# Optimization experiments

Hardware: AMD Instinct MI355X
Metric: run time of the kernel (lower is better)

## Reference

```python
import jax, jax.numpy as jnp
import numpy as np

H = 200  # LSTM units per layer
SEQ_LEN = 100
NUM_AXIS = 4


def setup_inputs() -> dict:
    key = jax.random.key(0)
    ks = jax.random.split(key, 12)
    B = 8192
    s = 0.05  # small init scale to avoid gate saturation
    inp = {
        "x": jax.random.normal(ks[0], (B, SEQ_LEN, 1), dtype=jnp.float32),
        # layer 0: input dim 1
        "W0": jax.random.normal(ks[1], (1, 4 * H), dtype=jnp.float32) * s,
        "U0": jax.random.normal(ks[2], (H, 4 * H), dtype=jnp.float32) * s,
        "b0": jax.random.normal(ks[3], (4 * H,), dtype=jnp.float32) * s,
        # layer 1
        "W1": jax.random.normal(ks[4], (H, 4 * H), dtype=jnp.float32) * s,
        "U1": jax.random.normal(ks[5], (H, 4 * H), dtype=jnp.float32) * s,
        "b1": jax.random.normal(ks[6], (4 * H,), dtype=jnp.float32) * s,
        # layer 2
        "W2": jax.random.normal(ks[7], (H, 4 * H), dtype=jnp.float32) * s,
        "U2": jax.random.normal(ks[8], (H, 4 * H), dtype=jnp.float32) * s,
        "b2": jax.random.normal(ks[9], (4 * H,), dtype=jnp.float32) * s,
        # dense head: 200 -> 400, tanh
        "Wfc": jax.random.normal(ks[10], (H, SEQ_LEN * NUM_AXIS), dtype=jnp.float32) * s,
        "bfc": jax.random.normal(ks[11], (SEQ_LEN * NUM_AXIS,), dtype=jnp.float32) * s,
    }
    return inp


def _lstm_step(h, c, xt, W, U, b):
    # Keras LSTMCell gate order: i, f, g(candidate), o
    z = xt @ W + h @ U + b  # [B, 4H]
    i, f, g, o = jnp.split(z, 4, axis=-1)
    c_new = jax.nn.sigmoid(f) * c + jax.nn.sigmoid(i) * jnp.tanh(g)
    h_new = jax.nn.sigmoid(o) * jnp.tanh(c_new)
    return h_new, c_new


def reference(x, W0, U0, b0, W1, U1, b1, W2, U2, b2, Wfc, bfc):
    B = x.shape[0]
    zeros = jnp.zeros((B, H), dtype=x.dtype)
    carry0 = (zeros, zeros, zeros, zeros, zeros, zeros)

    def step(carry, xt):
        h0, c0, h1, c1, h2, c2 = carry
        h0, c0 = _lstm_step(h0, c0, xt, W0, U0, b0)
        h1, c1 = _lstm_step(h1, c1, h0, W1, U1, b1)
        h2, c2 = _lstm_step(h2, c2, h1, W2, U2, b2)
        return (h0, c0, h1, c1, h2, c2), None

    # scan over time: x is [B, T, 1] -> [T, B, 1]
    xs = jnp.swapaxes(x, 0, 1)
    (h0, c0, h1, c1, h2, c2), _ = jax.lax.scan(step, carry0, xs)
    # return_sequences=False -> final top-layer hidden state
    y = jnp.tanh(h2 @ Wfc + bfc)  # [B, 400]
    return y.reshape(B, SEQ_LEN, NUM_AXIS)
```

## Files before the change

### kernel.cpp

```cpp
#include <hip/hip_runtime.h>

#define Hdim 200
#define NP   800
#define Tlen 100
#define BT   32
#define KB   7
#define HS   232
#define NT   50
#define THREADS 640
#define CH   5
#define CHSTR (NT*64*8)
#define MATSZ (KB*CHSTR)
#define SBUF  2560

#define WAIT_VM0   0x0F70
#define WAIT_VM5   0x0F75
#define WAIT_LGKM0 0xC07F

typedef float f32x4 __attribute__((ext_vector_type(4)));
typedef short s16x8 __attribute__((ext_vector_type(8)));

__device__ __forceinline__ ushort f2bf(float f) {
    unsigned u = __float_as_uint(f);
    return (ushort)((u + 0x7fffu + ((u >> 16) & 1u)) >> 16);
}
__device__ __forceinline__ float bf2f(ushort s) {
    return __uint_as_float(((unsigned)s) << 16);
}
__device__ __forceinline__ float sigmoid_fast(float v) {
    return 1.0f / (1.0f + __expf(-v));
}
__device__ __forceinline__ float tanh_fast(float v) {
    return 2.0f / (1.0f + __expf(-2.0f * v)) - 1.0f;
}
__device__ __forceinline__ void wg_barrier() {
    asm volatile("" ::: "memory");
    __builtin_amdgcn_s_waitcnt(WAIT_LGKM0);
    __builtin_amdgcn_s_barrier();
    asm volatile("" ::: "memory");
}

__global__ void pack_weights(const float* __restrict__ U0, const float* __restrict__ W1,
                             const float* __restrict__ U1, const float* __restrict__ W2,
                             const float* __restrict__ U2, ushort* __restrict__ dst) {
    int idx = blockIdx.x * blockDim.x + threadIdx.x;
    if (idx >= 5 * KB * NT * 64) return;
    int lane = idx & 63; int rest = idx >> 6;
    int nt = rest % NT; rest /= NT;
    int kb = rest % KB; int mi = rest / KB;
    const float* src = (mi == 0) ? U0 : (mi == 1) ? W1 : (mi == 2) ? U1 : (mi == 3) ? W2 : U2;
    int np = nt * 16 + (lane & 15);
    int ncol = (np & 3) * Hdim + (np >> 2);
    int k0 = kb * 32 + (lane >> 4) * 8;
    ushort v[8];
#pragma unroll
    for (int j = 0; j < 8; ++j) {
        int k = k0 + j;
        v[j] = (k < Hdim) ? f2bf(src[k * NP + ncol]) : (ushort)0;
    }
    uint4 o;
    o.x = (unsigned)v[0] | ((unsigned)v[1] << 16);
    o.y = (unsigned)v[2] | ((unsigned)v[3] << 16);
    o.z = (unsigned)v[4] | ((unsigned)v[5] << 16);
    o.w = (unsigned)v[6] | ((unsigned)v[7] << 16);
    ((uint4*)dst)[idx] = o;
}

__device__ __forceinline__ void stage_chunk(const ushort* gp, ushort* dstbuf, int lane) {
#pragma unroll
    for (int mt = 0; mt < CH; ++mt) {
        __builtin_amdgcn_global_load_lds(
            (const __attribute__((address_space(1))) void*)(gp + (size_t)mt * 512 + lane * 8),
            (__attribute__((address_space(3))) void*)(dstbuf + mt * 512),
            16, 0, 0);
    }
}

__device__ __forceinline__ void unpack4(const ushort* p, float (&o)[4]) {
    uint2 u = *(const uint2*)p;
    o[0] = bf2f((ushort)(u.x));  o[1] = bf2f((ushort)(u.x >> 16));
    o[2] = bf2f((ushort)(u.y));  o[3] = bf2f((ushort)(u.y >> 16));
}

__device__ __forceinline__ void gate_phase(f32x4 (&acc)[2][CH],
                                           float (&creg)[2][CH],
                                           ushort* __restrict__ hbl,
                                           int lane, int ct0) {
    const int l15 = lane & 15, q = lane >> 4;
#pragma unroll
    for (int nt = 0; nt < 2; ++nt) {
#pragma unroll
        for (int mt = 0; mt < CH; ++mt) {
            const int u = (ct0 + mt) * 4 + q;
            const int n = nt * 16 + l15;
            f32x4 z = acc[nt][mt];
            float iv = sigmoid_fast(z[0]);
            float fv = sigmoid_fast(z[1]);
            float gv = tanh_fast(z[2]);
            float ov = sigmoid_fast(z[3]);
            float c = fv * creg[nt][mt] + iv * gv;
            creg[nt][mt] = c;
            hbl[n * HS + u] = f2bf(ov * tanh_fast(c));
        }
    }
}

__global__ void __launch_bounds__(THREADS)
lstm3_mfma(const float* __restrict__ x,
           const float* __restrict__ W0, const float* __restrict__ b0,
           const float* __restrict__ b1, const float* __restrict__ b2,
           const float* __restrict__ Wfc, const float* __restrict__ bfc,
           const ushort* __restrict__ packed,
           float* __restrict__ out) {
    __shared__ ushort hb[3][BT][HS];
    __shared__ ushort stage[10][2][SBUF];
    __shared__ ushort pbwb[4][NP];
    __shared__ ushort xTs[Tlen][BT];
    __shared__ uint   gTab[35];
    __shared__ uint   bhTab[35];

    const int tid = threadIdx.x;
    const int wave = tid >> 6, lane = tid & 63;
    const int l15 = lane & 15, q = lane >> 4;
    const int ct0 = wave * CH;
    const int bx = blockIdx.x;
    const int bbase = bx * BT;

    for (int i = tid; i < 3 * BT * HS; i += THREADS) ((ushort*)hb)[i] = 0;
    for (int i = tid; i < NP; i += THREADS) {
        int nc = (i & 3) * Hdim + (i >> 2);
        pbwb[0][i] = f2bf(b0[nc]); pbwb[1][i] = f2bf(b1[nc]);
        pbwb[2][i] = f2bf(b2[nc]); pbwb[3][i] = f2bf(W0[nc]);
    }
    for (int i = tid; i < BT * Tlen; i += THREADS) {
        int m = i / Tlen, tt = i % Tlen;
        xTs[tt][m] = f2bf(x[(size_t)(bbase + m) * Tlen + tt]);
    }
    if (tid < 35) {
        int s = tid; uint goff, bhoff;
        if (s < 7) {
            int c = (s + bx) % 7;
            goff = 0u * MATSZ + c * CHSTR;           bhoff = 0u * BT * HS + c * 32;
        } else if (s < 21) {
            int c = (s - 7 + bx) % 14;
            if (c < 7) { goff = 2u * MATSZ + c * CHSTR;       bhoff = 1u * BT * HS + c * 32; }
            else       { goff = 1u * MATSZ + (c - 7) * CHSTR; bhoff = 0u * BT * HS + (c - 7) * 32; }
        } else {
            int c = (s - 21 + bx * 5) % 14;
            if (c < 7) { goff = 4u * MATSZ + c * CHSTR;       bhoff = 2u * BT * HS + c * 32; }
            else       { goff = 3u * MATSZ + (c - 7) * CHSTR; bhoff = 1u * BT * HS + (c - 7) * 32; }
        }
        gTab[s] = goff; bhTab[s] = bhoff;
    }
    __syncthreads();

    float creg[3][2][CH];
#pragma unroll
    for (int l = 0; l < 3; ++l)
#pragma unroll
        for (int nt = 0; nt < 2; ++nt)
#pragma unroll
            for (int mt = 0; mt < CH; ++mt) creg[l][nt][mt] = 0.0f;

    const ushort* pk = packed + (size_t)(ct0 * 64) * 8;
    ushort* sl = &stage[wave][0][0];
    ushort* hbflat = &hb[0][0][0];
    const int bhbase = l15 * HS + q * 8;

    stage_chunk(pk + gTab[0], sl, lane);
    stage_chunk(pk + gTab[1], sl + SBUF, lane);
    int isl = 2;

    for (int t = 0; t < Tlen; ++t) {
        f32x4 acc[2][CH];

        const float xn0 = bf2f(xTs[t][l15]);
        const float xn1 = bf2f(xTs[t][16 + l15]);
#pragma unroll
        for (int mt = 0; mt < CH; ++mt) {
            const int row = (ct0 + mt) * 16 + q * 4;
            float bb[4], ww[4];
            unpack4(&pbwb[0][row], bb);
            unpack4(&pbwb[3][row], ww);
#pragma unroll
            for (int r = 0; r < 4; ++r) {
                acc[0][mt][r] = fmaf(xn0, ww[r], bb[r]);
                acc[1][mt][r] = fmaf(xn1, ww[r], bb[r]);
            }
        }

#pragma unroll 1
        for (int s = 0; s < 7; ++s) {
            __builtin_amdgcn_s_waitcnt(WAIT_VM5);
            ushort* buf = sl + ((t + s) & 1) * SBUF;
            s16x8 frag[CH];
#pragma unroll
            for (int mt = 0; mt < CH; ++mt)
                frag[mt] = *(const s16x8*)(buf + mt * 512 + lane * 8);
            const ushort* bp = hbflat + bhTab[s] + bhbase;
            s16x8 bh0 = *(const s16x8*)bp;
            s16x8 bh1 = *(const s16x8*)(bp + 16 * HS);
#pragma unroll
            for (int mt = 0; mt < CH; ++mt) {
                acc[0][mt] = __builtin_amdgcn_mfma_f32_16x16x32_bf16(frag[mt], bh0, acc[0][mt], 0, 0, 0);
                acc[1][mt] = __builtin_amdgcn_mfma_f32_16x16x32_bf16(frag[mt], bh1, acc[1][mt], 0, 0, 0);
            }
            __builtin_amdgcn_s_waitcnt(WAIT_LGKM0);
            stage_chunk(pk + gTab[isl], buf, lane);
            isl = (isl == 34) ? 0 : isl + 1;
        }
        wg_barrier();
        gate_phase(acc, creg[0], hbflat + 0 * BT * HS, lane, ct0);
        wg_barrier();

#pragma unroll
        for (int mt = 0; mt < CH; ++mt) {
            const int row = (ct0 + mt) * 16 + q * 4;
            float bb[4];
            unpack4(&pbwb[1][row], bb);
#pragma unroll
            for (int r = 0; r < 4; ++r) { acc[0][mt][r] = bb[r]; acc[1][mt][r] = bb[r]; }
        }
#pragma unroll 1
        for (int s = 7; s < 21; ++s) {
            __builtin_amdgcn_s_waitcnt(WAIT_VM5);
            ushort* buf = sl + ((t + s) & 1) * SBUF;
            s16x8 frag[CH];
#pragma unroll
            for (int mt = 0; mt < CH; ++mt)
                frag[mt] = *(const s16x8*)(buf + mt * 512 + lane * 8);
            const ushort* bp = hbflat + bhTab[s] + bhbase;
            s16x8 bh0 = *(const s16x8*)bp;
            s16x8 bh1 = *(const s16x8*)(bp + 16 * HS);
#pragma unroll
            for (int mt = 0; mt < CH; ++mt) {
                acc[0][mt] = __builtin_amdgcn_mfma_f32_16x16x32_bf16(frag[mt], bh0, acc[0][mt], 0, 0, 0);
                acc[1][mt] = __builtin_amdgcn_mfma_f32_16x16x32_bf16(frag[mt], bh1, acc[1][mt], 0, 0, 0);
            }
            __builtin_amdgcn_s_waitcnt(WAIT_LGKM0);
            stage_chunk(pk + gTab[isl], buf, lane);
            isl = (isl == 34) ? 0 : isl + 1;
        }
        wg_barrier();
        gate_phase(acc, creg[1], hbflat + 1 * BT * HS, lane, ct0);
        wg_barrier();

#pragma unroll
        for (int mt = 0; mt < CH; ++mt) {
            const int row = (ct0 + mt) * 16 + q * 4;
            float bb[4];
            unpack4(&pbwb[2][row], bb);
#pragma unroll
            for (int r = 0; r < 4; ++r) { acc[0][mt][r] = bb[r]; acc[1][mt][r] = bb[r]; }
        }
#pragma unroll 1
        for (int s = 21; s < 35; ++s) {
            __builtin_amdgcn_s_waitcnt(WAIT_VM5);
            ushort* buf = sl + ((t + s) & 1) * SBUF;
            s16x8 frag[CH];
#pragma unroll
            for (int mt = 0; mt < CH; ++mt)
                frag[mt] = *(const s16x8*)(buf + mt * 512 + lane * 8);
            const ushort* bp = hbflat + bhTab[s] + bhbase;
            s16x8 bh0 = *(const s16x8*)bp;
            s16x8 bh1 = *(const s16x8*)(bp + 16 * HS);
#pragma unroll
            for (int mt = 0; mt < CH; ++mt) {
                acc[0][mt] = __builtin_amdgcn_mfma_f32_16x16x32_bf16(frag[mt], bh0, acc[0][mt], 0, 0, 0);
                acc[1][mt] = __builtin_amdgcn_mfma_f32_16x16x32_bf16(frag[mt], bh1, acc[1][mt], 0, 0, 0);
            }
            __builtin_amdgcn_s_waitcnt(WAIT_LGKM0);
            stage_chunk(pk + gTab[isl], buf, lane);
            isl = (isl == 34) ? 0 : isl + 1;
        }
        wg_barrier();
        gate_phase(acc, creg[2], hbflat + 2 * BT * HS, lane, ct0);
        wg_barrier();
    }
    __syncthreads();

    for (int gidx = tid; gidx < BT * 100; gidx += THREADS) {
        int m = gidx / 100;
        int j4 = (gidx % 100) * 4;
        const ushort* h2 = &hb[2][m][0];
        float4 a4 = *(const float4*)(bfc + j4);
        float s0 = a4.x, s1 = a4.y, s2 = a4.z, s3 = a4.w;
        for (int k = 0; k < Hdim; ++k) {
            float hk = bf2f(h2[k]);
            float4 w4 = *(const float4*)(Wfc + (size_t)k * 400 + j4);
            s0 = fmaf(hk, w4.x, s0);
            s1 = fmaf(hk, w4.y, s1);
            s2 = fmaf(hk, w4.z, s2);
            s3 = fmaf(hk, w4.w, s3);
        }
        float4 o4;
        o4.x = tanh_fast(s0); o4.y = tanh_fast(s1);
        o4.z = tanh_fast(s2); o4.w = tanh_fast(s3);
        *(float4*)(out + (size_t)(bbase + m) * 400 + j4) = o4;
    }
}

extern "C" void kernel_launch(void* const* d_in, const int* in_sizes, int n_in,
                              void* d_out, int out_size, void* d_ws, size_t ws_size,
                              hipStream_t stream) {
    const float* x   = (const float*)d_in[0];
    const float* W0  = (const float*)d_in[1];
    const float* U0  = (const float*)d_in[2];
    const float* b0  = (const float*)d_in[3];
    const float* W1  = (const float*)d_in[4];
    const float* U1  = (const float*)d_in[5];
    const float* b1  = (const float*)d_in[6];
    const float* W2  = (const float*)d_in[7];
    const float* U2  = (const float*)d_in[8];
    const float* b2  = (const float*)d_in[9];
    const float* Wfc = (const float*)d_in[10];
    const float* bfc = (const float*)d_in[11];
    float* out = (float*)d_out;
    ushort* packed = (ushort*)d_ws;

    const int B = in_sizes[0] / Tlen;
    const int pack_threads = 5 * KB * NT * 64;
    pack_weights<<<(pack_threads + 255) / 256, 256, 0, stream>>>(U0, W1, U1, W2, U2, packed);
    lstm3_mfma<<<B / BT, THREADS, 0, stream>>>(x, W0, b0, b1, b2, Wfc, bfc, packed, out);
}
```

Before: 2.798 ms.

## Load weight fragments directly into registers with double-buffered prefetch instead of LDS staging

Drops the global_load_lds staging buffers and the vmcnt waits. Each wave now loads its MFMA weight fragments straight from global memory into two register sets (fA/fB), prefetching two slots ahead. The slot loops are fully unrolled by template parity so the buffer choice is known at compile time. This frees a large amount of LDS and removes the LDS read step, but uses more VGPRs and leaves load latency to compiler-inserted waits.

```diff
diff --git a/kernel.cpp b/kernel.cpp
--- a/kernel.cpp
+++ b/kernel.cpp
@@ -11,10 +11,7 @@
 #define CH   5
 #define CHSTR (NT*64*8)
 #define MATSZ (KB*CHSTR)
-#define SBUF  2560
-
-#define WAIT_VM0   0x0F70
-#define WAIT_VM5   0x0F75
+
 #define WAIT_LGKM0 0xC07F
 
 typedef float f32x4 __attribute__((ext_vector_type(4)));
@@ -66,16 +63,6 @@
     ((uint4*)dst)[idx] = o;
 }
 
-__device__ __forceinline__ void stage_chunk(const ushort* gp, ushort* dstbuf, int lane) {
-#pragma unroll
-    for (int mt = 0; mt < CH; ++mt) {
-        __builtin_amdgcn_global_load_lds(
-            (const __attribute__((address_space(1))) void*)(gp + (size_t)mt * 512 + lane * 8),
-            (__attribute__((address_space(3))) void*)(dstbuf + mt * 512),
-            16, 0, 0);
-    }
-}
-
 __device__ __forceinline__ void unpack4(const ushort* p, float (&o)[4]) {
     uint2 u = *(const uint2*)p;
     o[0] = bf2f((ushort)(u.x));  o[1] = bf2f((ushort)(u.x >> 16));
@@ -105,6 +92,47 @@
     }
 }
 
+__device__ __forceinline__ void load_frags(s16x8 (&f)[CH],
+                                           const ushort* __restrict__ pkl, uint go) {
+    const ushort* gp = pkl + go;
+#pragma unroll
+    for (int mt = 0; mt < CH; ++mt)
+        f[mt] = *(const s16x8*)(gp + mt * 512);
+}
+
+__device__ __forceinline__ void slot_mfma(s16x8 (&f)[CH], f32x4 (&acc)[2][CH],
+                                          const ushort* hbp) {
+    s16x8 bh0 = *(const s16x8*)hbp;
+    s16x8 bh1 = *(const s16x8*)(hbp + 16 * HS);
+#pragma unroll
+    for (int mt = 0; mt < CH; ++mt) {
+        acc[0][mt] = __builtin_amdgcn_mfma_f32_16x16x32_bf16(f[mt], bh0, acc[0][mt], 0, 0, 0);
+        acc[1][mt] = __builtin_amdgcn_mfma_f32_16x16x32_bf16(f[mt], bh1, acc[1][mt], 0, 0, 0);
+    }
+}
+
+template<int PAR, int L>
+__device__ __forceinline__ void run_region(const int s0,
+        s16x8 (&fA)[CH], s16x8 (&fB)[CH], f32x4 (&acc)[2][CH],
+        const ushort* __restrict__ pkl,
+        const uint* gT, const uint* bhT,
+        const ushort* hbflat, const int bhbase) {
+#pragma unroll
+    for (int i = 0; i < L; ++i) {
+        const int s = s0 + i;
+        int gi = s + 2; if (gi >= 35) gi -= 35;
+        const ushort* hbp = hbflat + bhT[s] + bhbase;
+        const uint go = gT[gi];
+        if (((PAR + i) & 1) == 0) {
+            slot_mfma(fA, acc, hbp);
+            load_frags(fA, pkl, go);
+        } else {
+            slot_mfma(fB, acc, hbp);
+            load_frags(fB, pkl, go);
+        }
+    }
+}
+
 __global__ void __launch_bounds__(THREADS)
 lstm3_mfma(const float* __restrict__ x,
            const float* __restrict__ W0, const float* __restrict__ b0,
@@ -113,7 +141,6 @@
            const ushort* __restrict__ packed,
            float* __restrict__ out) {
     __shared__ ushort hb[3][BT][HS];
-    __shared__ ushort stage[10][2][SBUF];
     __shared__ ushort pbwb[4][NP];
     __shared__ ushort xTs[Tlen][BT];
     __shared__ uint   gTab[35];
@@ -162,14 +189,13 @@
 #pragma unroll
             for (int mt = 0; mt < CH; ++mt) creg[l][nt][mt] = 0.0f;
 
-    const ushort* pk = packed + (size_t)(ct0 * 64) * 8;
-    ushort* sl = &stage[wave][0][0];
+    const ushort* pkl = packed + ct0 * 512 + lane * 8;
     ushort* hbflat = &hb[0][0][0];
     const int bhbase = l15 * HS + q * 8;
 
-    stage_chunk(pk + gTab[0], sl, lane);
-    stage_chunk(pk + gTab[1], sl + SBUF, lane);
-    int isl = 2;
+    s16x8 fA[CH], fB[CH];
+    load_frags(fA, pkl, gTab[0]);
+    load_frags(fB, pkl, gTab[1]);
 
     for (int t = 0; t < Tlen; ++t) {
         f32x4 acc[2][CH];
@@ -189,26 +215,8 @@
             }
         }
 
-#pragma unroll 1
-        for (int s = 0; s < 7; ++s) {
-            __builtin_amdgcn_s_waitcnt(WAIT_VM5);
-            ushort* buf = sl + ((t + s) & 1) * SBUF;
-            s16x8 frag[CH];
-#pragma unroll
-            for (int mt = 0; mt < CH; ++mt)
-                frag[mt] = *(const s16x8*)(buf + mt * 512 + lane * 8);
-            const ushort* bp = hbflat + bhTab[s] + bhbase;
-            s16x8 bh0 = *(const s16x8*)bp;
-            s16x8 bh1 = *(const s16x8*)(bp + 16 * HS);
-#pragma unroll
-            for (int mt = 0; mt < CH; ++mt) {
-                acc[0][mt] = __builtin_amdgcn_mfma_f32_16x16x32_bf16(frag[mt], bh0, acc[0][mt], 0, 0, 0);
-                acc[1][mt] = __builtin_amdgcn_mfma_f32_16x16x32_bf16(frag[mt], bh1, acc[1][mt], 0, 0, 0);
-            }
-            __builtin_amdgcn_s_waitcnt(WAIT_LGKM0);
-            stage_chunk(pk + gTab[isl], buf, lane);
-            isl = (isl == 34) ? 0 : isl + 1;
-        }
+        if ((t & 1) == 0) run_region<0, 7>(0, fA, fB, acc, pkl, gTab, bhTab, hbflat, bhbase);
+        else              run_region<1, 7>(0, fA, fB, acc, pkl, gTab, bhTab, hbflat, bhbase);
         wg_barrier();
         gate_phase(acc, creg[0], hbflat + 0 * BT * HS, lane, ct0);
         wg_barrier();
@@ -221,26 +229,8 @@
 #pragma unroll
             for (int r = 0; r < 4; ++r) { acc[0][mt][r] = bb[r]; acc[1][mt][r] = bb[r]; }
         }
-#pragma unroll 1
-        for (int s = 7; s < 21; ++s) {
-            __builtin_amdgcn_s_waitcnt(WAIT_VM5);
-            ushort* buf = sl + ((t + s) & 1) * SBUF;
-            s16x8 frag[CH];
-#pragma unroll
-            for (int mt = 0; mt < CH; ++mt)
-                frag[mt] = *(const s16x8*)(buf + mt * 512 + lane * 8);
-            const ushort* bp = hbflat + bhTab[s] + bhbase;
-            s16x8 bh0 = *(const s16x8*)bp;
-            s16x8 bh1 = *(const s16x8*)(bp + 16 * HS);
-#pragma unroll
-            for (int mt = 0; mt < CH; ++mt) {
-                acc[0][mt] = __builtin_amdgcn_mfma_f32_16x16x32_bf16(frag[mt], bh0, acc[0][mt], 0, 0, 0);
-                acc[1][mt] = __builtin_amdgcn_mfma_f32_16x16x32_bf16(frag[mt], bh1, acc[1][mt], 0, 0, 0);
-            }
-            __builtin_amdgcn_s_waitcnt(WAIT_LGKM0);
-            stage_chunk(pk + gTab[isl], buf, lane);
-            isl = (isl == 34) ? 0 : isl + 1;
-        }
+        if ((t & 1) == 0) run_region<1, 14>(7, fA, fB, acc, pkl, gTab, bhTab, hbflat, bhbase);
+        else              run_region<0, 14>(7, fA, fB, acc, pkl, gTab, bhTab, hbflat, bhbase);
         wg_barrier();
         gate_phase(acc, creg[1], hbflat + 1 * BT * HS, lane, ct0);
         wg_barrier();
@@ -253,26 +243,8 @@
 #pragma unroll
             for (int r = 0; r < 4; ++r) { acc[0][mt][r] = bb[r]; acc[1][mt][r] = bb[r]; }
         }
-#pragma unroll 1
-        for (int s = 21; s < 35; ++s) {
-            __builtin_amdgcn_s_waitcnt(WAIT_VM5);
-            ushort* buf = sl + ((t + s) & 1) * SBUF;
-            s16x8 frag[CH];
-#pragma unroll
-            for (int mt = 0; mt < CH; ++mt)
-                frag[mt] = *(const s16x8*)(buf + mt * 512 + lane * 8);
-            const ushort* bp = hbflat + bhTab[s] + bhbase;
-            s16x8 bh0 = *(const s16x8*)bp;
-            s16x8 bh1 = *(const s16x8*)(bp + 16 * HS);
-#pragma unroll
-            for (int mt = 0; mt < CH; ++mt) {
-                acc[0][mt] = __builtin_amdgcn_mfma_f32_16x16x32_bf16(frag[mt], bh0, acc[0][mt], 0, 0, 0);
-                acc[1][mt] = __builtin_amdgcn_mfma_f32_16x16x32_bf16(frag[mt], bh1, acc[1][mt], 0, 0, 0);
-            }
-            __builtin_amdgcn_s_waitcnt(WAIT_LGKM0);
-            stage_chunk(pk + gTab[isl], buf, lane);
-            isl = (isl == 34) ? 0 : isl + 1;
-        }
+        if ((t & 1) == 0) run_region<1, 14>(21, fA, fB, acc, pkl, gTab, bhTab, hbflat, bhbase);
+        else              run_region<0, 14>(21, fA, fB, acc, pkl, gTab, bhTab, hbflat, bhbase);
         wg_barrier();
         gate_phase(acc, creg[2], hbflat + 2 * BT * HS, lane, ct0);
         wg_barrier();
```

Result: slower. 3.610 ms (+29.0%).

## Split W/U slot phases per layer to drop half the workgroup barriers

Applied to the files above, without the earlier changes.

Slots for layers 1 and 2 are reordered so the recurrent U·h_own chunks, which depend only on the previous step's state, run first. A single barrier then separates them from the input-projection chunks that read the freshly written lower-layer h. This lets the barrier that used to follow each gate phase be removed, cutting barriers per timestep from six to three and letting waves overlap gate math with the next layer's matmul work. It depends on careful read/write ordering of the shared hidden-state buffers, and the slot loop is factored into a helper.

```diff
diff --git a/kernel.cpp b/kernel.cpp
--- a/kernel.cpp
+++ b/kernel.cpp
@@ -13,7 +13,6 @@
 #define MATSZ (KB*CHSTR)
 #define SBUF  2560
 
-#define WAIT_VM0   0x0F70
 #define WAIT_VM5   0x0F75
 #define WAIT_LGKM0 0xC07F
 
@@ -105,6 +104,32 @@
     }
 }
 
+__device__ __forceinline__ void run_slots(int s0, int s1, int t,
+        ushort* __restrict__ sl, f32x4 (&acc)[2][CH],
+        const ushort* __restrict__ pk, const uint* gTab, const uint* bhTab,
+        const ushort* hbflat, int bhbase, int lane, int& isl) {
+#pragma unroll 1
+    for (int s = s0; s < s1; ++s) {
+        __builtin_amdgcn_s_waitcnt(WAIT_VM5);
+        ushort* buf = sl + ((t + s) & 1) * SBUF;
+        s16x8 frag[CH];
+#pragma unroll
+        for (int mt = 0; mt < CH; ++mt)
+            frag[mt] = *(const s16x8*)(buf + mt * 512 + lane * 8);
+        const ushort* bp = hbflat + bhTab[s] + bhbase;
+        s16x8 bh0 = *(const s16x8*)bp;
+        s16x8 bh1 = *(const s16x8*)(bp + 16 * HS);
+#pragma unroll
+        for (int mt = 0; mt < CH; ++mt) {
+            acc[0][mt] = __builtin_amdgcn_mfma_f32_16x16x32_bf16(frag[mt], bh0, acc[0][mt], 0, 0, 0);
+            acc[1][mt] = __builtin_amdgcn_mfma_f32_16x16x32_bf16(frag[mt], bh1, acc[1][mt], 0, 0, 0);
+        }
+        __builtin_amdgcn_s_waitcnt(WAIT_LGKM0);
+        stage_chunk(pk + gTab[isl], buf, lane);
+        isl = (isl == 34) ? 0 : isl + 1;
+    }
+}
+
 __global__ void __launch_bounds__(THREADS)
 lstm3_mfma(const float* __restrict__ x,
            const float* __restrict__ W0, const float* __restrict__ b0,
@@ -140,15 +165,19 @@
         int s = tid; uint goff, bhoff;
         if (s < 7) {
             int c = (s + bx) % 7;
-            goff = 0u * MATSZ + c * CHSTR;           bhoff = 0u * BT * HS + c * 32;
+            goff = 0u * MATSZ + c * CHSTR;  bhoff = 0u * BT * HS + c * 32;
+        } else if (s < 14) {
+            int c = (s - 7 + bx) % 7;
+            goff = 2u * MATSZ + c * CHSTR;  bhoff = 1u * BT * HS + c * 32;
         } else if (s < 21) {
-            int c = (s - 7 + bx) % 14;
-            if (c < 7) { goff = 2u * MATSZ + c * CHSTR;       bhoff = 1u * BT * HS + c * 32; }
-            else       { goff = 1u * MATSZ + (c - 7) * CHSTR; bhoff = 0u * BT * HS + (c - 7) * 32; }
+            int c = (s - 14 + bx) % 7;
+            goff = 1u * MATSZ + c * CHSTR;  bhoff = 0u * BT * HS + c * 32;
+        } else if (s < 28) {
+            int c = (s - 21 + bx * 5) % 7;
+            goff = 4u * MATSZ + c * CHSTR;  bhoff = 2u * BT * HS + c * 32;
         } else {
-            int c = (s - 21 + bx * 5) % 14;
-            if (c < 7) { goff = 4u * MATSZ + c * CHSTR;       bhoff = 2u * BT * HS + c * 32; }
-            else       { goff = 3u * MATSZ + (c - 7) * CHSTR; bhoff = 1u * BT * HS + (c - 7) * 32; }
+            int c = (s - 28 + bx * 5) % 7;
+            goff = 3u * MATSZ + c * CHSTR;  bhoff = 1u * BT * HS + c * 32;
         }
         gTab[s] = goff; bhTab[s] = bhoff;
     }
@@ -189,30 +218,10 @@
             }
         }
 
-#pragma unroll 1
-        for (int s = 0; s < 7; ++s) {
-            __builtin_amdgcn_s_waitcnt(WAIT_VM5);
-            ushort* buf = sl + ((t + s) & 1) * SBUF;
-            s16x8 frag[CH];
-#pragma unroll
-            for (int mt = 0; mt < CH; ++mt)
-                frag[mt] = *(const s16x8*)(buf + mt * 512 + lane * 8);
-            const ushort* bp = hbflat + bhTab[s] + bhbase;
-            s16x8 bh0 = *(const s16x8*)bp;
-            s16x8 bh1 = *(const s16x8*)(bp + 16 * HS);
-#pragma unroll
-            for (int mt = 0; mt < CH; ++mt) {
-                acc[0][mt] = __builtin_amdgcn_mfma_f32_16x16x32_bf16(frag[mt], bh0, acc[0][mt], 0, 0, 0);
-                acc[1][mt] = __builtin_amdgcn_mfma_f32_16x16x32_bf16(frag[mt], bh1, acc[1][mt], 0, 0, 0);
-            }
-            __builtin_amdgcn_s_waitcnt(WAIT_LGKM0);
-            stage_chunk(pk + gTab[isl], buf, lane);
-            isl = (isl == 34) ? 0 : isl + 1;
-        }
+        run_slots(0, 7, t, sl, acc, pk, gTab, bhTab, hbflat, bhbase, lane, isl);
         wg_barrier();
+
         gate_phase(acc, creg[0], hbflat + 0 * BT * HS, lane, ct0);
-        wg_barrier();
-
 #pragma unroll
         for (int mt = 0; mt < CH; ++mt) {
             const int row = (ct0 + mt) * 16 + q * 4;
@@ -221,30 +230,11 @@
 #pragma unroll
             for (int r = 0; r < 4; ++r) { acc[0][mt][r] = bb[r]; acc[1][mt][r] = bb[r]; }
         }
-#pragma unroll 1
-        for (int s = 7; s < 21; ++s) {
-            __builtin_amdgcn_s_waitcnt(WAIT_VM5);
-            ushort* buf = sl + ((t + s) & 1) * SBUF;
-            s16x8 frag[CH];
-#pragma unroll
-            for (int mt = 0; mt < CH; ++mt)
-                frag[mt] = *(const s16x8*)(buf + mt * 512 + lane * 8);
-            const ushort* bp = hbflat + bhTab[s] + bhbase;
-            s16x8 bh0 = *(const s16x8*)bp;
-            s16x8 bh1 = *(const s16x8*)(bp + 16 * HS);
-#pragma unroll
-            for (int mt = 0; mt < CH; ++mt) {
-                acc[0][mt] = __builtin_amdgcn_mfma_f32_16x16x32_bf16(frag[mt], bh0, acc[0][mt], 0, 0, 0);
-                acc[1][mt] = __builtin_amdgcn_mfma_f32_16x16x32_bf16(frag[mt], bh1, acc[1][mt], 0, 0, 0);
-            }
-            __builtin_amdgcn_s_waitcnt(WAIT_LGKM0);
-            stage_chunk(pk + gTab[isl], buf, lane);
-            isl = (isl == 34) ? 0 : isl + 1;
-        }
+        run_slots(7, 14, t, sl, acc, pk, gTab, bhTab, hbflat, bhbase, lane, isl);
         wg_barrier();
+
+        run_slots(14, 21, t, sl, acc, pk, gTab, bhTab, hbflat, bhbase, lane, isl);
         gate_phase(acc, creg[1], hbflat + 1 * BT * HS, lane, ct0);
-        wg_barrier();
-
 #pragma unroll
         for (int mt = 0; mt < CH; ++mt) {
             const int row = (ct0 + mt) * 16 + q * 4;
@@ -253,29 +243,11 @@
 #pragma unroll
             for (int r = 0; r < 4; ++r) { acc[0][mt][r] = bb[r]; acc[1][mt][r] = bb[r]; }
         }
-#pragma unroll 1
-        for (int s = 21; s < 35; ++s) {
-            __builtin_amdgcn_s_waitcnt(WAIT_VM5);
-            ushort* buf = sl + ((t + s) & 1) * SBUF;
-            s16x8 frag[CH];
-#pragma unroll
-            for (int mt = 0; mt < CH; ++mt)
-                frag[mt] = *(const s16x8*)(buf + mt * 512 + lane * 8);
-            const ushort* bp = hbflat + bhTab[s] + bhbase;
-            s16x8 bh0 = *(const s16x8*)bp;
-            s16x8 bh1 = *(const s16x8*)(bp + 16 * HS);
-#pragma unroll
-            for (int mt = 0; mt < CH; ++mt) {
-                acc[0][mt] = __builtin_amdgcn_mfma_f32_16x16x32_bf16(frag[mt], bh0, acc[0][mt], 0, 0, 0);
-                acc[1][mt] = __builtin_amdgcn_mfma_f32_16x16x32_bf16(frag[mt], bh1, acc[1][mt], 0, 0, 0);
-            }
-            __builtin_amdgcn_s_waitcnt(WAIT_LGKM0);
-            stage_chunk(pk + gTab[isl], buf, lane);
-            isl = (isl == 34) ? 0 : isl + 1;
-        }
+        run_slots(21, 28, t, sl, acc, pk, gTab, bhTab, hbflat, bhbase, lane, isl);
         wg_barrier();
+
+        run_slots(28, 35, t, sl, acc, pk, gTab, bhTab, hbflat, bhbase, lane, isl);
         gate_phase(acc, creg[2], hbflat + 2 * BT * HS, lane, ct0);
-        wg_barrier();
     }
     __syncthreads();
 
```

Result: no change. 2.829 ms (+1.1%).

## Split weight slots between direct register loads and LDS-staged DMA chunks

Applied to the files above, without the earlier changes.

Each wave now alternates weight slots. Every other slot's fragments are loaded directly from global memory into registers, and the rest go through the double-buffered LDS staging path with a lookahead of four slots. This halves LDS staging traffic and the ds_read work per timestep, and lets direct loads overlap the MFMAs of the staged slot. In exchange it adds register pressure for the extra fragments, exposes global load latency on the direct slots, and complicates the slot-to-buffer indexing.

```diff
diff --git a/kernel.cpp b/kernel.cpp
--- a/kernel.cpp
+++ b/kernel.cpp
@@ -13,7 +13,6 @@
 #define MATSZ (KB*CHSTR)
 #define SBUF  2560
 
-#define WAIT_VM0   0x0F70
 #define WAIT_VM5   0x0F75
 #define WAIT_LGKM0 0xC07F
 
@@ -105,6 +104,61 @@
     }
 }
 
+__device__ __forceinline__ void mfma10(const s16x8 (&f)[CH], f32x4 (&acc)[2][CH],
+                                       const ushort* bp) {
+    s16x8 bh0 = *(const s16x8*)bp;
+    s16x8 bh1 = *(const s16x8*)(bp + 16 * HS);
+#pragma unroll
+    for (int mt = 0; mt < CH; ++mt) {
+        acc[0][mt] = __builtin_amdgcn_mfma_f32_16x16x32_bf16(f[mt], bh0, acc[0][mt], 0, 0, 0);
+        acc[1][mt] = __builtin_amdgcn_mfma_f32_16x16x32_bf16(f[mt], bh1, acc[1][mt], 0, 0, 0);
+    }
+}
+
+__device__ __forceinline__ void dma_slot(int s, bool issue_next, s16x8 (&fd)[CH],
+        f32x4 (&acc)[2][CH], ushort* sl, const ushort* pk, const ushort* pkl,
+        const uint* gTab, const uint* bhTab, const ushort* hbflat, int bhbase, int lane) {
+    __builtin_amdgcn_s_waitcnt(WAIT_VM5);
+    ushort* buf = sl + ((s >> 1) & 1) * SBUF;
+    if (issue_next) {
+        const ushort* gp = pkl + gTab[s + 1];
+#pragma unroll
+        for (int mt = 0; mt < CH; ++mt)
+            fd[mt] = *(const s16x8*)(gp + mt * 512);
+    }
+    s16x8 frag[CH];
+#pragma unroll
+    for (int mt = 0; mt < CH; ++mt)
+        frag[mt] = *(const s16x8*)(buf + mt * 512 + lane * 8);
+    mfma10(frag, acc, hbflat + bhTab[s] + bhbase);
+    __builtin_amdgcn_s_waitcnt(WAIT_LGKM0);
+    int rs = s + 4; if (rs >= 36) rs -= 36;
+    stage_chunk(pk + gTab[rs], buf, lane);
+}
+
+__device__ __forceinline__ void dir_slot(int s, const s16x8 (&fd)[CH], f32x4 (&acc)[2][CH],
+        const uint* bhTab, const ushort* hbflat, int bhbase) {
+    mfma10(fd, acc, hbflat + bhTab[s] + bhbase);
+}
+
+template<bool FRESH>
+__device__ __forceinline__ void run_pairs(int s0, int n, s16x8 (&fd)[CH],
+        f32x4 (&acc)[2][CH], ushort* sl, const ushort* pk, const ushort* pkl,
+        const uint* gTab, const uint* bhTab, const ushort* hbflat, int bhbase, int lane) {
+    if (FRESH) {
+        const ushort* gp = pkl + gTab[s0];
+#pragma unroll
+        for (int mt = 0; mt < CH; ++mt)
+            fd[mt] = *(const s16x8*)(gp + mt * 512);
+    }
+#pragma unroll 1
+    for (int i = 0; i < n; ++i) {
+        int s = s0 + 2 * i;
+        dir_slot(s, fd, acc, bhTab, hbflat, bhbase);
+        dma_slot(s + 1, i != n - 1, fd, acc, sl, pk, pkl, gTab, bhTab, hbflat, bhbase, lane);
+    }
+}
+
 __global__ void __launch_bounds__(THREADS)
 lstm3_mfma(const float* __restrict__ x,
            const float* __restrict__ W0, const float* __restrict__ b0,
@@ -162,14 +216,16 @@
 #pragma unroll
             for (int mt = 0; mt < CH; ++mt) creg[l][nt][mt] = 0.0f;
 
-    const ushort* pk = packed + (size_t)(ct0 * 64) * 8;
+    const ushort* pk  = packed + (size_t)(ct0 * 64) * 8;
+    const ushort* pkl = pk + lane * 8;
     ushort* sl = &stage[wave][0][0];
     ushort* hbflat = &hb[0][0][0];
     const int bhbase = l15 * HS + q * 8;
 
     stage_chunk(pk + gTab[0], sl, lane);
-    stage_chunk(pk + gTab[1], sl + SBUF, lane);
-    int isl = 2;
+    stage_chunk(pk + gTab[2], sl + SBUF, lane);
+
+    s16x8 fd[CH];
 
     for (int t = 0; t < Tlen; ++t) {
         f32x4 acc[2][CH];
@@ -189,26 +245,8 @@
             }
         }
 
-#pragma unroll 1
-        for (int s = 0; s < 7; ++s) {
-            __builtin_amdgcn_s_waitcnt(WAIT_VM5);
-            ushort* buf = sl + ((t + s) & 1) * SBUF;
-            s16x8 frag[CH];
-#pragma unroll
-            for (int mt = 0; mt < CH; ++mt)
-                frag[mt] = *(const s16x8*)(buf + mt * 512 + lane * 8);
-            const ushort* bp = hbflat + bhTab[s] + bhbase;
-            s16x8 bh0 = *(const s16x8*)bp;
-            s16x8 bh1 = *(const s16x8*)(bp + 16 * HS);
-#pragma unroll
-            for (int mt = 0; mt < CH; ++mt) {
-                acc[0][mt] = __builtin_amdgcn_mfma_f32_16x16x32_bf16(frag[mt], bh0, acc[0][mt], 0, 0, 0);
-                acc[1][mt] = __builtin_amdgcn_mfma_f32_16x16x32_bf16(frag[mt], bh1, acc[1][mt], 0, 0, 0);
-            }
-            __builtin_amdgcn_s_waitcnt(WAIT_LGKM0);
-            stage_chunk(pk + gTab[isl], buf, lane);
-            isl = (isl == 34) ? 0 : isl + 1;
-        }
+        dma_slot(0, true, fd, acc, sl, pk, pkl, gTab, bhTab, hbflat, bhbase, lane);
+        run_pairs<false>(1, 3, fd, acc, sl, pk, pkl, gTab, bhTab, hbflat, bhbase, lane);
         wg_barrier();
         gate_phase(acc, creg[0], hbflat + 0 * BT * HS, lane, ct0);
         wg_barrier();
@@ -221,26 +259,7 @@
 #pragma unroll
             for (int r = 0; r < 4; ++r) { acc[0][mt][r] = bb[r]; acc[1][mt][r] = bb[r]; }
         }
-#pragma unroll 1
-        for (int s = 7; s < 21; ++s) {
-            __builtin_amdgcn_s_waitcnt(WAIT_VM5);
-            ushort* buf = sl + ((t + s) & 1) * SBUF;
-            s16x8 frag[CH];
-#pragma unroll
-            for (int mt = 0; mt < CH; ++mt)
-                frag[mt] = *(const s16x8*)(buf + mt * 512 + lane * 8);
-            const ushort* bp = hbflat + bhTab[s] + bhbase;
-            s16x8 bh0 = *(const s16x8*)bp;
-            s16x8 bh1 = *(const s16x8*)(bp + 16 * HS);
-#pragma unroll
-            for (int mt = 0; mt < CH; ++mt) {
-                acc[0][mt] = __builtin_amdgcn_mfma_f32_16x16x32_bf16(frag[mt], bh0, acc[0][mt], 0, 0, 0);
-                acc[1][mt] = __builtin_amdgcn_mfma_f32_16x16x32_bf16(frag[mt], bh1, acc[1][mt], 0, 0, 0);
-            }
-            __builtin_amdgcn_s_waitcnt(WAIT_LGKM0);
-            stage_chunk(pk + gTab[isl], buf, lane);
-            isl = (isl == 34) ? 0 : isl + 1;
-        }
+        run_pairs<true>(7, 7, fd, acc, sl, pk, pkl, gTab, bhTab, hbflat, bhbase, lane);
         wg_barrier();
         gate_phase(acc, creg[1], hbflat + 1 * BT * HS, lane, ct0);
         wg_barrier();
@@ -253,26 +272,7 @@
 #pragma unroll
             for (int r = 0; r < 4; ++r) { acc[0][mt][r] = bb[r]; acc[1][mt][r] = bb[r]; }
         }
-#pragma unroll 1
-        for (int s = 21; s < 35; ++s) {
-            __builtin_amdgcn_s_waitcnt(WAIT_VM5);
-            ushort* buf = sl + ((t + s) & 1) * SBUF;
-            s16x8 frag[CH];
-#pragma unroll
-            for (int mt = 0; mt < CH; ++mt)
-                frag[mt] = *(const s16x8*)(buf + mt * 512 + lane * 8);
-            const ushort* bp = hbflat + bhTab[s] + bhbase;
-            s16x8 bh0 = *(const s16x8*)bp;
-            s16x8 bh1 = *(const s16x8*)(bp + 16 * HS);
-#pragma unroll
-            for (int mt = 0; mt < CH; ++mt) {
-                acc[0][mt] = __builtin_amdgcn_mfma_f32_16x16x32_bf16(frag[mt], bh0, acc[0][mt], 0, 0, 0);
-                acc[1][mt] = __builtin_amdgcn_mfma_f32_16x16x32_bf16(frag[mt], bh1, acc[1][mt], 0, 0, 0);
-            }
-            __builtin_amdgcn_s_waitcnt(WAIT_LGKM0);
-            stage_chunk(pk + gTab[isl], buf, lane);
-            isl = (isl == 34) ? 0 : isl + 1;
-        }
+        run_pairs<true>(21, 7, fd, acc, sl, pk, pkl, gTab, bhTab, hbflat, bhbase, lane);
         wg_barrier();
         gate_phase(acc, creg[2], hbflat + 2 * BT * HS, lane, ct0);
         wg_barrier();
```

After: 2.869 ms. 2.5% more time.
